# Optimization experiments

Measured on AMD Instinct MI355X. Metric: run time of the kernel, lower is better.

The kernel has to match this reference:

```python
import jax, jax.numpy as jnp
import numpy as np

T, C, H, K = 32768, 64, 256, 10
N_LAYERS = 2


def _init(key, shape, scale):
    return jax.random.uniform(key, shape, minval=-scale, maxval=scale, dtype=jnp.float32)


def setup_inputs() -> dict:
    key = jax.random.key(0)
    ks = jax.random.split(key, 32)
    d = {"x": jax.random.normal(ks[0], (T, C), dtype=jnp.float32)}
    i = 1
    in_sz = C
    for l in range(N_LAYERS):
        s = 1.0 / np.sqrt(H)
        for dn in ("f", "b"):
            d[f"w_ih_{dn}{l}"] = _init(ks[i], (3 * H, in_sz), s); i += 1
            d[f"w_hh_{dn}{l}"] = _init(ks[i], (3 * H, H), s); i += 1
            d[f"b_{dn}{l}"] = _init(ks[i], (3 * H,), s); i += 1
            d[f"bn_{dn}{l}"] = _init(ks[i], (H,), s); i += 1
        in_sz = 2 * H
    s2 = 1.0 / np.sqrt(2 * H)
    d["mu_w"] = _init(ks[i], (K, 2 * H), s2); i += 1
    d["mu_b"] = _init(ks[i], (K,), s2); i += 1
    d["sg_w"] = _init(ks[i], (K, 2 * H), s2); i += 1
    d["sg_b"] = _init(ks[i], (K,), s2); i += 1
    return d


def _gru(xs, w_ih, w_hh, b, bn, reverse):
    # Equinox GRUCell math: r,z,n gate order, bias_n added inside r-gated term.
    # Input projections for all timesteps are batched into one GEMM (same math).
    i_all = xs @ w_ih.T + b  # (T, 3H)
    h0 = jnp.zeros(w_hh.shape[1], xs.dtype)

    def step(h, i_t):
        hr, hz, hg = jnp.split(w_hh @ h, 3)
        ir, iz, ig = jnp.split(i_t, 3)
        r = jax.nn.sigmoid(ir + hr)
        z = jax.nn.sigmoid(iz + hz)
        g = jnp.tanh(ig + r * (hg + bn))
        h_new = (1 - z) * g + z * h
        return h_new, h_new

    # reverse=True == scanning xs[::-1] then flipping outputs (original code).
    _, out = jax.lax.scan(step, h0, i_all, reverse=reverse)
    return out  # (T, H)


def reference(x, w_ih_f0, w_hh_f0, b_f0, bn_f0, w_ih_b0, w_hh_b0, b_b0, bn_b0,
              w_ih_f1, w_hh_f1, b_f1, bn_f1, w_ih_b1, w_hh_b1, b_b1, bn_b1,
              mu_w, mu_b, sg_w, sg_b):
    layers = [
        ((w_ih_f0, w_hh_f0, b_f0, bn_f0), (w_ih_b0, w_hh_b0, b_b0, bn_b0)),
        ((w_ih_f1, w_hh_f1, b_f1, bn_f1), (w_ih_b1, w_hh_b1, b_b1, bn_b1)),
    ]
    h = x
    for (pf, pb) in layers:
        out_f = _gru(h, *pf, reverse=False)
        out_b = _gru(h, *pb, reverse=True)
        h = jnp.concatenate([out_f, out_b], axis=-1)  # (T, 2H)
    mu = h @ mu_w.T + mu_b                       # (T, K)
    sigma = jax.nn.softplus(h @ sg_w.T + sg_b)   # (T, K)
    return (mu, sigma)
```

## Files before the change

kernel.cpp:

```cpp
#include <hip/hip_runtime.h>
#include <hip/hip_fp16.h>


typedef _Float16 f16x8 __attribute__((ext_vector_type(8)));
typedef float    f32x4 __attribute__((ext_vector_type(4)));

#define T_LEN 32768
#define HDIM  256

__global__ void cvt_x_kernel(const float* __restrict__ x, __half* __restrict__ xh) {
    int i = (blockIdx.x * 256 + threadIdx.x) * 8;
    f32x4 a = *reinterpret_cast<const f32x4*>(x + i);
    f32x4 b = *reinterpret_cast<const f32x4*>(x + i + 4);
    f16x8 v;
#pragma unroll
    for (int j = 0; j < 4; ++j) { v[j] = (_Float16)a[j]; v[4 + j] = (_Float16)b[j]; }
    *reinterpret_cast<f16x8*>(xh + i) = v;
}

__global__ __launch_bounds__(256, 1)
void gemm_f16_kernel(const __half* __restrict__ A,
                     const float* __restrict__ B0, const float* __restrict__ B1,
                     __half* __restrict__ C0, __half* __restrict__ C1, int K) {
    const float* B = blockIdx.z ? B1 : B0;
    __half*      C = blockIdx.z ? C1 : C0;
    const int m0 = blockIdx.x * 128, n0 = blockIdx.y * 128;
    const int tid = threadIdx.x, lane = tid & 63, wv = tid >> 6;
    const int wm = (wv >> 1) * 64, wn = (wv & 1) * 64;
    const int qq = lane >> 4, r16 = lane & 15;

    __shared__ __align__(16) _Float16 As[128][40];
    __shared__ __align__(16) _Float16 Bs[128][40];

    f32x4 acc[4][4];
#pragma unroll
    for (int i = 0; i < 4; ++i)
#pragma unroll
        for (int j = 0; j < 4; ++j) acc[i][j] = (f32x4){0.f, 0.f, 0.f, 0.f};

    const int r = tid >> 1, seg = tid & 1;
    for (int k0 = 0; k0 < K; k0 += 32) {
        const f16x8* ap = reinterpret_cast<const f16x8*>(A + (size_t)(m0 + r) * K + k0 + 16 * seg);
        f16x8 a0 = ap[0], a1 = ap[1];
        const f32x4* bp = reinterpret_cast<const f32x4*>(B + (size_t)(n0 + r) * K + k0 + 16 * seg);
        f32x4 b0v = bp[0], b1v = bp[1], b2v = bp[2], b3v = bp[3];
        f16x8 bh0, bh1;
#pragma unroll
        for (int j = 0; j < 4; ++j) {
            bh0[j] = (_Float16)b0v[j]; bh0[4 + j] = (_Float16)b1v[j];
            bh1[j] = (_Float16)b2v[j]; bh1[4 + j] = (_Float16)b3v[j];
        }
        *reinterpret_cast<f16x8*>(&As[r][16 * seg])     = a0;
        *reinterpret_cast<f16x8*>(&As[r][16 * seg + 8]) = a1;
        *reinterpret_cast<f16x8*>(&Bs[r][16 * seg])     = bh0;
        *reinterpret_cast<f16x8*>(&Bs[r][16 * seg + 8]) = bh1;
        __syncthreads();

        f16x8 af[4], bf[4];
#pragma unroll
        for (int mi = 0; mi < 4; ++mi)
            af[mi] = *reinterpret_cast<const f16x8*>(&As[wm + 16 * mi + r16][8 * qq]);
#pragma unroll
        for (int ni = 0; ni < 4; ++ni)
            bf[ni] = *reinterpret_cast<const f16x8*>(&Bs[wn + 16 * ni + r16][8 * qq]);
#pragma unroll
        for (int mi = 0; mi < 4; ++mi)
#pragma unroll
            for (int ni = 0; ni < 4; ++ni)
                acc[mi][ni] = __builtin_amdgcn_mfma_f32_16x16x32_f16(af[mi], bf[ni], acc[mi][ni], 0, 0, 0);
        __syncthreads();
    }
#pragma unroll
    for (int mi = 0; mi < 4; ++mi)
#pragma unroll
        for (int ni = 0; ni < 4; ++ni)
#pragma unroll
            for (int rr = 0; rr < 4; ++rr) {
                int grow = m0 + wm + 16 * mi + 4 * qq + rr;
                int gcol = n0 + wn + 16 * ni + r16;
                C[(size_t)grow * 768 + gcol] = __float2half(acc[mi][ni][rr]);
            }
}

__global__ __launch_bounds__(512, 1)
void recur_kernel(const float* __restrict__ whh_f, const float* __restrict__ whh_b,
                  const float* __restrict__ b_f,  const float* __restrict__ b_b,
                  const float* __restrict__ bn_f, const float* __restrict__ bn_b,
                  const __half* __restrict__ iall_f, const __half* __restrict__ iall_b,
                  __half* __restrict__ out ) {
    const int dir = blockIdx.x;
    const float*  whh  = dir ? whh_b  : whh_f;
    const float*  bb   = dir ? b_b    : b_f;
    const float*  bn   = dir ? bn_b   : bn_f;
    const __half* iall = dir ? iall_b : iall_f;
    const int colofs   = dir ? HDIM : 0;

    const int tid = threadIdx.x;
    const int lane = tid & 63;
    const int wv = tid >> 6;
    const int qq = lane >> 4;
    const int r16 = lane & 15;

    __shared__ __align__(16) __half hbuf[2][HDIM];
    __shared__ __align__(16) float  pre[768];

    f16x8 a[6][8];
#pragma unroll
    for (int i = 0; i < 6; ++i) {
        int row = 16 * (6 * wv + i) + r16;
        const float* wr = whh + (size_t)row * HDIM + 8 * qq;
#pragma unroll
        for (int kc = 0; kc < 8; ++kc) {
            const f32x4* p4 = reinterpret_cast<const f32x4*>(wr + 32 * kc);
            f32x4 w0 = p4[0], w1 = p4[1];
            f16x8 v;
#pragma unroll
            for (int j = 0; j < 4; ++j) { v[j] = (_Float16)w0[j]; v[4 + j] = (_Float16)w1[j]; }
            a[i][kc] = v;
        }
    }
    float cbr = 0.f, cbz = 0.f, cbg = 0.f, cbn = 0.f, hold = 0.f;
    if (tid < HDIM) {
        cbr = bb[tid]; cbz = bb[HDIM + tid]; cbg = bb[2 * HDIM + tid]; cbn = bn[tid];
        hbuf[0][tid] = __float2half(0.f);
    }
    __syncthreads();

    for (int ts = 0; ts < T_LEN; ++ts) {
        const int tp  = dir ? (T_LEN - 1 - ts) : ts;
        const int cur = ts & 1, nxt = cur ^ 1;

        float xr = 0.f, xz = 0.f, xg = 0.f;
        if (tid < HDIM) {
            const __half* ip = iall + (size_t)tp * 768;
            xr = __half2float(ip[tid]);
            xz = __half2float(ip[HDIM + tid]);
            xg = __half2float(ip[2 * HDIM + tid]);
        }

        f16x8 bf[8];
        const __half* hb = hbuf[cur];
#pragma unroll
        for (int kc = 0; kc < 8; ++kc)
            bf[kc] = *reinterpret_cast<const f16x8*>(hb + kc * 32 + qq * 8);

        f32x4 acc[6];
#pragma unroll
        for (int i = 0; i < 6; ++i) acc[i] = (f32x4){0.f, 0.f, 0.f, 0.f};
#pragma unroll
        for (int kc = 0; kc < 8; ++kc)
#pragma unroll
            for (int i = 0; i < 6; ++i)
                acc[i] = __builtin_amdgcn_mfma_f32_16x16x32_f16(a[i][kc], bf[kc], acc[i], 0, 0, 0);

        if (r16 == 0) {
#pragma unroll
            for (int i = 0; i < 6; ++i) {
                int rowb = 16 * (6 * wv + i) + 4 * qq;
                *reinterpret_cast<f32x4*>(pre + rowb) = acc[i];
            }
        }
        __syncthreads();

        if (tid < HDIM) {
            float pr = pre[tid], pz = pre[HDIM + tid], pg = pre[2 * HDIM + tid];
            float ar = xr + cbr + pr;
            float az = xz + cbz + pz;
            float rg = 1.f / (1.f + __expf(-ar));
            float zg = 1.f / (1.f + __expf(-az));
            float ag = xg + cbg + rg * (pg + cbn);
            float e2 = __expf(-2.f * fabsf(ag));
            float th = (1.f - e2) / (1.f + e2);
            float gg = (ag >= 0.f) ? th : -th;
            float hn = (1.f - zg) * gg + zg * hold;
            hold = hn;
            __half hh = __float2half(hn);
            hbuf[nxt][tid] = hh;
            out[(size_t)tp * 512 + colofs + tid] = hh;
        }
        __syncthreads();
    }
}

__device__ inline float softplus_f(float x) {
    return (x > 20.f) ? x : log1pf(__expf(x));
}

__global__ __launch_bounds__(256, 1)
void head_kernel(const __half* __restrict__ h1,
                 const float* __restrict__ mu_w, const float* __restrict__ mu_b,
                 const float* __restrict__ sg_w, const float* __restrict__ sg_b,
                 float* __restrict__ outp) {
    const int tid = threadIdx.x, lane = tid & 63, wv = tid >> 6;
    const int qq = lane >> 4, r16 = lane & 15;
    const int m0 = blockIdx.x * 128;

    __shared__ __align__(16) _Float16 Ws[32][520];
    __shared__ __align__(16) _Float16 Hs[128][40];

    {
        int rw = tid >> 3, c0 = (tid & 7) * 64;
        const float* src = (rw < 10) ? (mu_w + (size_t)rw * 512 + c0)
                         : (rw < 20) ? (sg_w + (size_t)(rw - 10) * 512 + c0) : nullptr;
        for (int cc = 0; cc < 64; cc += 8) {
            f16x8 hv;
            if (src) {
                f32x4 v0 = *reinterpret_cast<const f32x4*>(src + cc);
                f32x4 v1 = *reinterpret_cast<const f32x4*>(src + cc + 4);
#pragma unroll
                for (int j = 0; j < 4; ++j) { hv[j] = (_Float16)v0[j]; hv[4 + j] = (_Float16)v1[j]; }
            } else {
#pragma unroll
                for (int j = 0; j < 8; ++j) hv[j] = (_Float16)0.f;
            }
            *reinterpret_cast<f16x8*>(&Ws[rw][c0 + cc]) = hv;
        }
    }
    __syncthreads();

    f32x4 acc[2][2];
#pragma unroll
    for (int i = 0; i < 2; ++i)
#pragma unroll
        for (int j = 0; j < 2; ++j) acc[i][j] = (f32x4){0.f, 0.f, 0.f, 0.f};

    const int r = tid >> 1, seg = tid & 1;
    for (int kc = 0; kc < 16; ++kc) {
        const f16x8* hp = reinterpret_cast<const f16x8*>(h1 + (size_t)(m0 + r) * 512 + kc * 32 + 16 * seg);
        f16x8 h0 = hp[0], h1v = hp[1];
        *reinterpret_cast<f16x8*>(&Hs[r][16 * seg])     = h0;
        *reinterpret_cast<f16x8*>(&Hs[r][16 * seg + 8]) = h1v;
        __syncthreads();
        f16x8 af[2], bf[2];
#pragma unroll
        for (int mi = 0; mi < 2; ++mi)
            af[mi] = *reinterpret_cast<const f16x8*>(&Hs[wv * 32 + 16 * mi + r16][8 * qq]);
#pragma unroll
        for (int ni = 0; ni < 2; ++ni)
            bf[ni] = *reinterpret_cast<const f16x8*>(&Ws[16 * ni + r16][kc * 32 + 8 * qq]);
#pragma unroll
        for (int mi = 0; mi < 2; ++mi)
#pragma unroll
            for (int ni = 0; ni < 2; ++ni)
                acc[mi][ni] = __builtin_amdgcn_mfma_f32_16x16x32_f16(af[mi], bf[ni], acc[mi][ni], 0, 0, 0);
        __syncthreads();
    }

#pragma unroll
    for (int mi = 0; mi < 2; ++mi)
#pragma unroll
        for (int ni = 0; ni < 2; ++ni) {
            int ch = 16 * ni + r16;
#pragma unroll
            for (int rr = 0; rr < 4; ++rr) {
                int grow = m0 + wv * 32 + 16 * mi + 4 * qq + rr;
                float v = acc[mi][ni][rr];
                if (ch < 10) {
                    outp[(size_t)grow * 10 + ch] = v + mu_b[ch];
                } else if (ch < 20) {
                    outp[(size_t)T_LEN * 10 + (size_t)grow * 10 + (ch - 10)] = softplus_f(v + sg_b[ch - 10]);
                }
            }
        }
}

extern "C" void kernel_launch(void* const* d_in, const int* in_sizes, int n_in,
                              void* d_out, int out_size, void* d_ws, size_t ws_size,
                              hipStream_t stream) {
    const float* x      = (const float*)d_in[0];
    const float* wih_f0 = (const float*)d_in[1];
    const float* whh_f0 = (const float*)d_in[2];
    const float* b_f0   = (const float*)d_in[3];
    const float* bn_f0  = (const float*)d_in[4];
    const float* wih_b0 = (const float*)d_in[5];
    const float* whh_b0 = (const float*)d_in[6];
    const float* b_b0   = (const float*)d_in[7];
    const float* bn_b0  = (const float*)d_in[8];
    const float* wih_f1 = (const float*)d_in[9];
    const float* whh_f1 = (const float*)d_in[10];
    const float* b_f1   = (const float*)d_in[11];
    const float* bn_f1  = (const float*)d_in[12];
    const float* wih_b1 = (const float*)d_in[13];
    const float* whh_b1 = (const float*)d_in[14];
    const float* b_b1   = (const float*)d_in[15];
    const float* bn_b1  = (const float*)d_in[16];
    const float* mu_w   = (const float*)d_in[17];
    const float* mu_b   = (const float*)d_in[18];
    const float* sg_w   = (const float*)d_in[19];
    const float* sg_b   = (const float*)d_in[20];

    char* ws = (char*)d_ws;
    __half* xh     = (__half*)(ws);
    __half* iall_f = (__half*)(ws + (size_t)4 * 1024 * 1024);
    __half* iall_b = (__half*)(ws + (size_t)52 * 1024 * 1024);
    __half* out0   = (__half*)(ws + (size_t)100 * 1024 * 1024);
    __half* out1   = (__half*)(ws + (size_t)132 * 1024 * 1024);

    cvt_x_kernel<<<dim3((T_LEN * 64) / (256 * 8)), 256, 0, stream>>>(x, xh);
    gemm_f16_kernel<<<dim3(T_LEN / 128, 6, 2), 256, 0, stream>>>(xh, wih_f0, wih_b0, iall_f, iall_b, 64);
    recur_kernel<<<dim3(2), 512, 0, stream>>>(whh_f0, whh_b0, b_f0, b_b0, bn_f0, bn_b0, iall_f, iall_b, out0);
    gemm_f16_kernel<<<dim3(T_LEN / 128, 6, 2), 256, 0, stream>>>(out0, wih_f1, wih_b1, iall_f, iall_b, 512);
    recur_kernel<<<dim3(2), 512, 0, stream>>>(whh_f1, whh_b1, b_f1, b_b1, bn_f1, bn_b1, iall_f, iall_b, out1);
    head_kernel<<<dim3(T_LEN / 128), 256, 0, stream>>>(out1, mu_w, mu_b, sg_w, sg_b, (float*)d_out);
}
```

Before: 84.43 ms.

## Shrink GRU recurrence to 256 threads, prefetch inputs, fold bias into GEMM

Result: slower. 102.8 ms (+21.8%).

```diff
diff --git a/kernel.cpp b/kernel.cpp
--- a/kernel.cpp
+++ b/kernel.cpp
@@ -21,9 +21,11 @@
 __global__ __launch_bounds__(256, 1)
 void gemm_f16_kernel(const __half* __restrict__ A,
                      const float* __restrict__ B0, const float* __restrict__ B1,
+                     const float* __restrict__ bias0, const float* __restrict__ bias1,
                      __half* __restrict__ C0, __half* __restrict__ C1, int K) {
-    const float* B = blockIdx.z ? B1 : B0;
-    __half*      C = blockIdx.z ? C1 : C0;
+    const float* B    = blockIdx.z ? B1 : B0;
+    const float* bias = blockIdx.z ? bias1 : bias0;
+    __half*      C    = blockIdx.z ? C1 : C0;
     const int m0 = blockIdx.x * 128, n0 = blockIdx.y * 128;
     const int tid = threadIdx.x, lane = tid & 63, wv = tid >> 6;
     const int wm = (wv >> 1) * 64, wn = (wv & 1) * 64;
@@ -78,19 +80,65 @@
             for (int rr = 0; rr < 4; ++rr) {
                 int grow = m0 + wm + 16 * mi + 4 * qq + rr;
                 int gcol = n0 + wn + 16 * ni + r16;
-                C[(size_t)grow * 768 + gcol] = __float2half(acc[mi][ni][rr]);
+                C[(size_t)grow * 768 + gcol] = __float2half(acc[mi][ni][rr] + bias[gcol]);
             }
 }
 
-__global__ __launch_bounds__(512, 1)
+#define LOAD_X(TP, XR, XZ, XG)                                   \
+    {                                                            \
+        const __half* ip = iall + (size_t)(TP) * 768;            \
+        XR = ip[tid]; XZ = ip[256 + tid]; XG = ip[512 + tid];    \
+    }
+
+#define GRU_STEP(P, XR, XZ, XG, TP)                                              \
+    {                                                                            \
+        const __half* hb = hbuf[P];                                              \
+        f16x8 bf[8];                                                             \
+        _Pragma("unroll")                                                        \
+        for (int kc = 0; kc < 8; ++kc)                                           \
+            bf[kc] = *reinterpret_cast<const f16x8*>(hb + kc * 32 + qq * 8);     \
+        f32x4 acc[12];                                                           \
+        _Pragma("unroll")                                                        \
+        for (int i = 0; i < 12; ++i) acc[i] = (f32x4){0.f, 0.f, 0.f, 0.f};       \
+        _Pragma("unroll")                                                        \
+        for (int kc = 0; kc < 8; ++kc)                                           \
+            _Pragma("unroll")                                                    \
+            for (int i = 0; i < 12; ++i)                                         \
+                acc[i] = __builtin_amdgcn_mfma_f32_16x16x32_f16(a[i][kc], bf[kc], acc[i], 0, 0, 0); \
+        if (r16 == 0) {                                                          \
+            _Pragma("unroll")                                                    \
+            for (int i = 0; i < 12; ++i)                                         \
+                *reinterpret_cast<f32x4*>(pre + 16 * (12 * wv + i) + 4 * qq) = acc[i]; \
+        }                                                                        \
+        asm volatile("s_waitcnt lgkmcnt(0)" ::: "memory");                       \
+        __builtin_amdgcn_s_barrier();                                            \
+        {                                                                        \
+            float pr = pre[tid], pz = pre[256 + tid], pg = pre[512 + tid];       \
+            float ar = __half2float(XR) + pr;                                    \
+            float az = __half2float(XZ) + pz;                                    \
+            float rg = 1.f / (1.f + __expf(-ar));                                \
+            float zg = 1.f / (1.f + __expf(-az));                                \
+            float ag = __half2float(XG) + rg * (pg + cbn);                       \
+            float e2 = __expf(-2.f * fabsf(ag));                                 \
+            float th = (1.f - e2) / (1.f + e2);                                  \
+            float gg = (ag >= 0.f) ? th : -th;                                   \
+            float hn = (1.f - zg) * gg + zg * hold;                              \
+            hold = hn;                                                           \
+            __half hh = __float2half(hn);                                        \
+            hbuf[(P) ^ 1][tid] = hh;                                             \
+            out[(size_t)(TP) * 512 + colofs + tid] = hh;                         \
+        }                                                                        \
+        asm volatile("s_waitcnt lgkmcnt(0)" ::: "memory");                       \
+        __builtin_amdgcn_s_barrier();                                            \
+    }
+
+__global__ __launch_bounds__(256, 1)
 void recur_kernel(const float* __restrict__ whh_f, const float* __restrict__ whh_b,
-                  const float* __restrict__ b_f,  const float* __restrict__ b_b,
                   const float* __restrict__ bn_f, const float* __restrict__ bn_b,
                   const __half* __restrict__ iall_f, const __half* __restrict__ iall_b,
                   __half* __restrict__ out ) {
     const int dir = blockIdx.x;
     const float*  whh  = dir ? whh_b  : whh_f;
-    const float*  bb   = dir ? b_b    : b_f;
     const float*  bn   = dir ? bn_b   : bn_f;
     const __half* iall = dir ? iall_b : iall_f;
     const int colofs   = dir ? HDIM : 0;
@@ -104,10 +152,10 @@
     __shared__ __align__(16) __half hbuf[2][HDIM];
     __shared__ __align__(16) float  pre[768];
 
-    f16x8 a[6][8];
-#pragma unroll
-    for (int i = 0; i < 6; ++i) {
-        int row = 16 * (6 * wv + i) + r16;
+    f16x8 a[12][8];
+#pragma unroll
+    for (int i = 0; i < 12; ++i) {
+        int row = 16 * (12 * wv + i) + r16;
         const float* wr = whh + (size_t)row * HDIM + 8 * qq;
 #pragma unroll
         for (int kc = 0; kc < 8; ++kc) {
@@ -119,66 +167,24 @@
             a[i][kc] = v;
         }
     }
-    float cbr = 0.f, cbz = 0.f, cbg = 0.f, cbn = 0.f, hold = 0.f;
-    if (tid < HDIM) {
-        cbr = bb[tid]; cbz = bb[HDIM + tid]; cbg = bb[2 * HDIM + tid]; cbn = bn[tid];
-        hbuf[0][tid] = __float2half(0.f);
-    }
+    float cbn = bn[tid];
+    float hold = 0.f;
+    hbuf[0][tid] = __float2half(0.f);
     __syncthreads();
 
-    for (int ts = 0; ts < T_LEN; ++ts) {
-        const int tp  = dir ? (T_LEN - 1 - ts) : ts;
-        const int cur = ts & 1, nxt = cur ^ 1;
-
-        float xr = 0.f, xz = 0.f, xg = 0.f;
-        if (tid < HDIM) {
-            const __half* ip = iall + (size_t)tp * 768;
-            xr = __half2float(ip[tid]);
-            xz = __half2float(ip[HDIM + tid]);
-            xg = __half2float(ip[2 * HDIM + tid]);
-        }
-
-        f16x8 bf[8];
-        const __half* hb = hbuf[cur];
-#pragma unroll
-        for (int kc = 0; kc < 8; ++kc)
-            bf[kc] = *reinterpret_cast<const f16x8*>(hb + kc * 32 + qq * 8);
-
-        f32x4 acc[6];
-#pragma unroll
-        for (int i = 0; i < 6; ++i) acc[i] = (f32x4){0.f, 0.f, 0.f, 0.f};
-#pragma unroll
-        for (int kc = 0; kc < 8; ++kc)
-#pragma unroll
-            for (int i = 0; i < 6; ++i)
-                acc[i] = __builtin_amdgcn_mfma_f32_16x16x32_f16(a[i][kc], bf[kc], acc[i], 0, 0, 0);
-
-        if (r16 == 0) {
-#pragma unroll
-            for (int i = 0; i < 6; ++i) {
-                int rowb = 16 * (6 * wv + i) + 4 * qq;
-                *reinterpret_cast<f32x4*>(pre + rowb) = acc[i];
-            }
-        }
-        __syncthreads();
-
-        if (tid < HDIM) {
-            float pr = pre[tid], pz = pre[HDIM + tid], pg = pre[2 * HDIM + tid];
-            float ar = xr + cbr + pr;
-            float az = xz + cbz + pz;
-            float rg = 1.f / (1.f + __expf(-ar));
-            float zg = 1.f / (1.f + __expf(-az));
-            float ag = xg + cbg + rg * (pg + cbn);
-            float e2 = __expf(-2.f * fabsf(ag));
-            float th = (1.f - e2) / (1.f + e2);
-            float gg = (ag >= 0.f) ? th : -th;
-            float hn = (1.f - zg) * gg + zg * hold;
-            hold = hn;
-            __half hh = __float2half(hn);
-            hbuf[nxt][tid] = hh;
-            out[(size_t)tp * 512 + colofs + tid] = hh;
-        }
-        __syncthreads();
+    __half xr0, xz0, xg0, xr1, xz1, xg1;
+    LOAD_X(dir ? T_LEN - 1 : 0, xr0, xz0, xg0);
+
+    for (int ts = 0; ts < T_LEN; ts += 2) {
+        const int tp0 = dir ? (T_LEN - 1 - ts) : ts;
+        const int tp1 = dir ? (T_LEN - 2 - ts) : ts + 1;
+        const int ts2 = (ts + 2 < T_LEN) ? ts + 2 : ts + 1;
+        const int tp2 = dir ? (T_LEN - 1 - ts2) : ts2;
+
+        LOAD_X(tp1, xr1, xz1, xg1);
+        GRU_STEP(0, xr0, xz0, xg0, tp0);
+        LOAD_X(tp2, xr0, xz0, xg0);
+        GRU_STEP(1, xr1, xz1, xg1, tp1);
     }
 }
 
@@ -297,9 +303,9 @@
     __half* out1   = (__half*)(ws + (size_t)132 * 1024 * 1024);
 
     cvt_x_kernel<<<dim3((T_LEN * 64) / (256 * 8)), 256, 0, stream>>>(x, xh);
-    gemm_f16_kernel<<<dim3(T_LEN / 128, 6, 2), 256, 0, stream>>>(xh, wih_f0, wih_b0, iall_f, iall_b, 64);
-    recur_kernel<<<dim3(2), 512, 0, stream>>>(whh_f0, whh_b0, b_f0, b_b0, bn_f0, bn_b0, iall_f, iall_b, out0);
-    gemm_f16_kernel<<<dim3(T_LEN / 128, 6, 2), 256, 0, stream>>>(out0, wih_f1, wih_b1, iall_f, iall_b, 512);
-    recur_kernel<<<dim3(2), 512, 0, stream>>>(whh_f1, whh_b1, b_f1, b_b1, bn_f1, bn_b1, iall_f, iall_b, out1);
+    gemm_f16_kernel<<<dim3(T_LEN / 128, 6, 2), 256, 0, stream>>>(xh, wih_f0, wih_b0, b_f0, b_b0, iall_f, iall_b, 64);
+    recur_kernel<<<dim3(2), 256, 0, stream>>>(whh_f0, whh_b0, bn_f0, bn_b0, iall_f, iall_b, out0);
+    gemm_f16_kernel<<<dim3(T_LEN / 128, 6, 2), 256, 0, stream>>>(out0, wih_f1, wih_b1, b_f1, b_b1, iall_f, iall_b, 512);
+    recur_kernel<<<dim3(2), 256, 0, stream>>>(whh_f1, whh_b1, bn_f1, bn_b1, iall_f, iall_b, out1);
     head_kernel<<<dim3(T_LEN / 128), 256, 0, stream>>>(out1, mu_w, mu_b, sg_w, sg_b, (float*)d_out);
 }
```
